# Performance work log

Hardware: AMD Instinct MI355X
Metric: run time of the kernel (lower is better)

## Reference

```python
import jax, jax.numpy as jnp
import numpy as np

M_FEATS = 1536      # number of proposals (docstring: [M, K])
K_DIM = 128         # feature dim per docstring example
NUM_CLASSES = 16    # label vocabulary; torch.unique loop becomes a fixed class sweep


def setup_inputs() -> dict:
    key = jax.random.key(0)
    k1, k2 = jax.random.split(key)
    features = jax.random.normal(k1, (M_FEATS, K_DIM), dtype=jnp.float32)
    labels = jax.random.randint(k2, (M_FEATS,), 0, NUM_CLASSES, dtype=jnp.int32)
    # ious all ones -> keep = (ious >= 0.5) is all-True, so the boolean filter is identity
    ious = jnp.ones((M_FEATS,), dtype=jnp.float32)
    return {"features": features, "labels": labels, "ious": ious}


def reference(features, labels, ious):
    # reweight_func='none' -> coef = ones_like(ious); keep mask is all-True by construction
    coef = jnp.ones_like(ious)
    # similarity [M, M]; coef broadcasts over columns, matching `similarity * coef` in torch
    sim = jnp.matmul(features, features.T) * coef[None, :]
    m = sim.shape[0]
    eye = jnp.eye(m, dtype=sim.dtype)
    # ground set term: logdet(similarity + 0.5 I)  (mask_ground is all ones)
    ground = jnp.linalg.slogdet(sim + 0.5 * eye)[1]

    # Per-label logdet of the submatrix S_c + 0.5 I_{n_c}. Instead of extracting a
    # variable-size submatrix (not jit-able), embed it in a full [M, M] matrix that is
    # block-diagonal: class block = S_c + 0.5 I, off-class diagonal = 1. Its logdet
    # equals logdet(S_c + 0.5 I). Absent classes give identity -> logdet 0, matching
    # torch.unique skipping them.
    onehot = (labels[:, None] == jnp.arange(NUM_CLASSES, dtype=labels.dtype)[None, :])
    onehot = onehot.astype(sim.dtype)  # [M, C]

    def class_logdet(mask):  # mask: [M] 0/1 indicator for one class
        A = sim * (mask[:, None] * mask[None, :]) + jnp.diag(0.5 * mask + (1.0 - mask))
        return jnp.linalg.slogdet(A)[1]

    per_class = jax.vmap(class_logdet)(onehot.T)  # [C]
    loss = jnp.sum(per_class) - ground
    return loss  # scalar; .mean() of a scalar is itself
```

## Files before the change

### kernel.cpp

```cpp
#include <hip/hip_runtime.h>
#include <math.h>


#define M_FEATS 1536
#define K_DIM 128
#define NUM_CLASSES 16
#define SLICE 96
#define GRAM_ELEMS (K_DIM * K_DIM)
#define PIDX(i) ((i) + ((i) >> 4))
#define SENT 0x13579BDF
#define MP 104

typedef short bf16x8 __attribute__((ext_vector_type(8)));
typedef float f32x4 __attribute__((ext_vector_type(4)));

__device__ __forceinline__ short f2bf(float x) {
    unsigned u = __float_as_uint(x);
    u += 0x7FFFu + ((u >> 16) & 1u);
    return (short)(u >> 16);
}

__device__ __forceinline__ void gram_mfma(
    const float* __restrict__ f, const int* list, int n, int contig_base,
    short* FT, float* __restrict__ gout, int t)
{
    const int wave = t >> 6, lane = t & 63, ln = lane & 15, quad = lane >> 4;
    const int mlane = t & 31, cgrp = t >> 5;

    f32x4 acc[2][8];
#pragma unroll
    for (int x = 0; x < 2; ++x)
#pragma unroll
        for (int tc = 0; tc < 8; ++tc)
            acc[x][tc] = (f32x4){0.f, 0.f, 0.f, 0.f};

    const int nchunks = (n + 95) / 96;
    for (int ch = 0; ch < nchunks; ++ch) {
        const int cb = ch * 96;
#pragma unroll
        for (int it = 0; it < 12; ++it) {
            const int m = (it % 3) * 32 + mlane;
            const int cg = (it / 3) * 8 + cgrp;
            const int gm = cb + m;
            float4 v = make_float4(0.f, 0.f, 0.f, 0.f);
            if (gm < n) {
                const int src = list ? list[gm] : (contig_base + gm);
                v = *(const float4*)(f + (size_t)src * K_DIM + cg * 4);
            }
            FT[(cg * 4 + 0) * MP + m] = f2bf(v.x);
            FT[(cg * 4 + 1) * MP + m] = f2bf(v.y);
            FT[(cg * 4 + 2) * MP + m] = f2bf(v.z);
            FT[(cg * 4 + 3) * MP + m] = f2bf(v.w);
        }
        __syncthreads();
#pragma unroll
        for (int kc = 0; kc < 3; ++kc) {
            const int kb = kc * 32 + quad * 8;
            bf16x8 a0 = *(const bf16x8*)(FT + ((wave * 2 + 0) * 16 + ln) * MP + kb);
            bf16x8 a1 = *(const bf16x8*)(FT + ((wave * 2 + 1) * 16 + ln) * MP + kb);
#pragma unroll
            for (int tc = 0; tc < 8; ++tc) {
                bf16x8 bb = *(const bf16x8*)(FT + (tc * 16 + ln) * MP + kb);
                acc[0][tc] = __builtin_amdgcn_mfma_f32_16x16x32_bf16(
                    a0, bb, acc[0][tc], 0, 0, 0);
                acc[1][tc] = __builtin_amdgcn_mfma_f32_16x16x32_bf16(
                    a1, bb, acc[1][tc], 0, 0, 0);
            }
        }
        __syncthreads();
    }

#pragma unroll
    for (int x = 0; x < 2; ++x)
#pragma unroll
        for (int tc = 0; tc < 8; ++tc)
#pragma unroll
            for (int rr = 0; rr < 4; ++rr)
                gout[((wave * 2 + x) * 16 + quad * 4 + rr) * K_DIM + tc * 16 + ln]
                    = acc[x][tc][rr];
}

__device__ __forceinline__ float chol128(
    float A[8][8], const int t, const int rg, const int cg,
    const int i0, const int j0,
    float4* panLo, float4* panHi, float4* wshLo, float4* wshHi, float* logp)
{
    if (rg == 0) {
#pragma unroll
        for (int q = 0; q < 8; ++q) {
            panLo[PIDX(j0 + q)] = make_float4(A[0][q], A[1][q], A[2][q], A[3][q]);
            panHi[PIDX(j0 + q)] = make_float4(A[4][q], A[5][q], A[6][q], A[7][q]);
        }
    }

#pragma unroll 1
    for (int s = 0; s < 16; ++s) {
        const int k = 8 * s;
        __syncthreads();

        if (t < K_DIM) {
            float4 dL[8], dH[8];
#pragma unroll
            for (int c = 0; c < 8; ++c) {
                dL[c] = panLo[PIDX(k + c)];
                dH[c] = panHi[PIDX(k + c)];
            }
            float4 aL = panLo[PIDX(t)], aH = panHi[PIDX(t)];

            float D[8][8];
#pragma unroll
            for (int c = 0; c < 8; ++c) {
                D[0][c] = dL[c].x; D[1][c] = dL[c].y;
                D[2][c] = dL[c].z; D[3][c] = dL[c].w;
                D[4][c] = dH[c].x; D[5][c] = dH[c].y;
                D[6][c] = dH[c].z; D[7][c] = dH[c].w;
            }

            float L[8][8], ic[8];
            float prod = 1.0f;
#pragma unroll
            for (int c = 0; c < 8; ++c) {
                float v = D[c][c];
#pragma unroll
                for (int m = 0; m < c; ++m) v = fmaf(-L[c][m], L[c][m], v);
                prod *= v;
                ic[c] = rsqrtf(v);
#pragma unroll
                for (int r = c + 1; r < 8; ++r) {
                    float x = D[r][c];
#pragma unroll
                    for (int m = 0; m < c; ++m) x = fmaf(-L[r][m], L[c][m], x);
                    L[r][c] = x * ic[c];
                }
            }
            if (t == 0) logp[s] = prod;

            float a[8] = {aL.x, aL.y, aL.z, aL.w, aH.x, aH.y, aH.z, aH.w};
            float w[8];
#pragma unroll
            for (int c = 0; c < 8; ++c) {
                float x = a[c];
#pragma unroll
                for (int m = 0; m < c; ++m) x = fmaf(-L[c][m], w[m], x);
                w[c] = x * ic[c];
            }
            wshLo[PIDX(t)] = make_float4(w[0], w[1], w[2], w[3]);
            wshHi[PIDX(t)] = make_float4(w[4], w[5], w[6], w[7]);
        }
        __syncthreads();

        if (rg > s && cg > s) {
            float4 wrL[8], wrH[8];
#pragma unroll
            for (int r = 0; r < 8; ++r) {
                wrL[r] = wshLo[PIDX(i0 + r)];
                wrH[r] = wshHi[PIDX(i0 + r)];
            }
#pragma unroll
            for (int q = 0; q < 8; ++q) {
                float4 wjL = wshLo[PIDX(j0 + q)];
                float4 wjH = wshHi[PIDX(j0 + q)];
#pragma unroll
                for (int r = 0; r < 8; ++r) {
                    float x = A[r][q];
                    x = fmaf(-wrL[r].x, wjL.x, x);
                    x = fmaf(-wrL[r].y, wjL.y, x);
                    x = fmaf(-wrL[r].z, wjL.z, x);
                    x = fmaf(-wrL[r].w, wjL.w, x);
                    x = fmaf(-wrH[r].x, wjH.x, x);
                    x = fmaf(-wrH[r].y, wjH.y, x);
                    x = fmaf(-wrH[r].z, wjH.z, x);
                    x = fmaf(-wrH[r].w, wjH.w, x);
                    A[r][q] = x;
                }
            }
        }
        if (rg == s + 1) {
#pragma unroll
            for (int q = 0; q < 8; ++q) {
                panLo[PIDX(j0 + q)] = make_float4(A[0][q], A[1][q], A[2][q], A[3][q]);
                panHi[PIDX(j0 + q)] = make_float4(A[4][q], A[5][q], A[6][q], A[7][q]);
            }
        }
    }

    float ls = 0.0f;
    if (t == 0) {
#pragma unroll
        for (int s = 0; s < 16; ++s) ls += logf(logp[s]);
    }
    return ls;
}

__global__ __launch_bounds__(256, 1) void fused_kernel(
    const float* __restrict__ f, const int* __restrict__ labels,
    float* __restrict__ partials, float* __restrict__ groundG,
    float* __restrict__ cgrams,
    int* __restrict__ flag1, int* __restrict__ flag2,
    float* __restrict__ ldet, int* __restrict__ flag3,
    float* __restrict__ out)
{
    __shared__ int cnt;
    __shared__ int list[M_FEATS];
    __shared__ short FT[K_DIM * MP];
    __shared__ float4 panLo[136], panHi[136], wshLo[136], wshHi[136];
    __shared__ float logp[16];

    const int b = blockIdx.x;
    const int t = threadIdx.x;
    const int rg = t >> 4;
    const int cg = t & 15;
    const int i0 = rg << 3;
    const int j0 = cg << 3;

    float A[8][8];

    if (b < NUM_CLASSES) {
        gram_mfma(f, nullptr, SLICE, SLICE * b, FT,
                  partials + (size_t)b * GRAM_ELEMS, t);
        __syncthreads();
        if (t == 0)
            __hip_atomic_store(&flag1[b], SENT, __ATOMIC_RELEASE,
                               __HIP_MEMORY_SCOPE_AGENT);

        if (t < NUM_CLASSES)
            while (__hip_atomic_load(&flag1[t], __ATOMIC_ACQUIRE,
                                     __HIP_MEMORY_SCOPE_AGENT) != SENT)
                __builtin_amdgcn_s_sleep(2);
        __syncthreads();

        {
            const int row = 8 * b + (t >> 5);
            const int col = (t & 31) << 2;
            float4 s = make_float4(0.f, 0.f, 0.f, 0.f);
#pragma unroll
            for (int c = 0; c < NUM_CLASSES; ++c) {
                float4 v = *(const float4*)(partials + (size_t)c * GRAM_ELEMS
                                            + row * K_DIM + col);
                s.x += v.x; s.y += v.y; s.z += v.z; s.w += v.w;
            }
            *(float4*)(groundG + row * K_DIM + col) = s;
        }
        __syncthreads();
        if (t == 0)
            __hip_atomic_store(&flag2[b], SENT, __ATOMIC_RELEASE,
                               __HIP_MEMORY_SCOPE_AGENT);
        return;
    }

    if (b < 2 * NUM_CLASSES) {
        const int cls = b - NUM_CLASSES;
        if (t == 0) cnt = 0;
        __syncthreads();
        {
            const int lane = t & 63;
            const unsigned long long ltmask = (lane == 63)
                ? 0x7FFFFFFFFFFFFFFFull : ((1ull << lane) - 1ull);
#pragma unroll
            for (int it = 0; it < M_FEATS / 256; ++it) {
                const int i = it * 256 + t;
                const bool pred = (labels[i] == cls);
                const unsigned long long mask = __ballot(pred);
                int base = 0;
                if (lane == 0 && mask)
                    base = atomicAdd(&cnt, __popcll(mask));
                base = __shfl(base, 0);
                if (pred)
                    list[base + __popcll(mask & ltmask)] = i;
            }
        }
        __syncthreads();
        const int n = cnt;

        float* g = cgrams + (size_t)cls * GRAM_ELEMS;
        gram_mfma(f, list, n, 0, FT, g, t);
        __syncthreads();

#pragma unroll
        for (int r = 0; r < 8; ++r) {
            float4 v0 = *(const float4*)(g + (i0 + r) * K_DIM + j0);
            float4 v1 = *(const float4*)(g + (i0 + r) * K_DIM + j0 + 4);
            A[r][0] = v0.x; A[r][1] = v0.y; A[r][2] = v0.z; A[r][3] = v0.w;
            A[r][4] = v1.x; A[r][5] = v1.y; A[r][6] = v1.z; A[r][7] = v1.w;
        }
#pragma unroll
        for (int r = 0; r < 8; ++r)
#pragma unroll
            for (int q = 0; q < 8; ++q)
                if ((i0 + r) == (j0 + q)) A[r][q] += 0.5f;

        float ls = chol128(A, t, rg, cg, i0, j0, panLo, panHi, wshLo, wshHi, logp);

        if (t == 0) {
            ldet[cls] = ls;
            __hip_atomic_store(&flag3[cls], SENT, __ATOMIC_RELEASE,
                               __HIP_MEMORY_SCOPE_AGENT);
        }
        return;
    }

    if (t < NUM_CLASSES)
        while (__hip_atomic_load(&flag2[t], __ATOMIC_ACQUIRE,
                                 __HIP_MEMORY_SCOPE_AGENT) != SENT)
            __builtin_amdgcn_s_sleep(2);
    __syncthreads();

#pragma unroll
    for (int r = 0; r < 8; ++r) {
        float4 v0 = *(const float4*)(groundG + (i0 + r) * K_DIM + j0);
        float4 v1 = *(const float4*)(groundG + (i0 + r) * K_DIM + j0 + 4);
        A[r][0] = v0.x; A[r][1] = v0.y; A[r][2] = v0.z; A[r][3] = v0.w;
        A[r][4] = v1.x; A[r][5] = v1.y; A[r][6] = v1.z; A[r][7] = v1.w;
    }
#pragma unroll
    for (int r = 0; r < 8; ++r)
#pragma unroll
        for (int q = 0; q < 8; ++q)
            if ((i0 + r) == (j0 + q)) A[r][q] += 0.5f;

    float ls = chol128(A, t, rg, cg, i0, j0, panLo, panHi, wshLo, wshHi, logp);

    if (t < NUM_CLASSES)
        while (__hip_atomic_load(&flag3[t], __ATOMIC_ACQUIRE,
                                 __HIP_MEMORY_SCOPE_AGENT) != SENT)
            __builtin_amdgcn_s_sleep(2);
    __syncthreads();

    if (t == 0) {
        float total = 1920.0f * 0.6931471805599453f - ls;
#pragma unroll
        for (int c = 0; c < NUM_CLASSES; ++c) total += ldet[c];
        out[0] = total;
    }
}

extern "C" void kernel_launch(void* const* d_in, const int* in_sizes, int n_in,
                              void* d_out, int out_size, void* d_ws, size_t ws_size,
                              hipStream_t stream)
{
    const float* features = (const float*)d_in[0];
    const int* labels = (const int*)d_in[1];

    float* partials = (float*)d_ws;
    float* groundG  = partials + (size_t)NUM_CLASSES * GRAM_ELEMS;
    float* cgrams   = groundG + GRAM_ELEMS;
    int* flag1      = (int*)(cgrams + (size_t)NUM_CLASSES * GRAM_ELEMS);
    int* flag2      = flag1 + NUM_CLASSES;
    float* ldetp    = (float*)(flag2 + NUM_CLASSES);
    int* flag3      = (int*)(ldetp + NUM_CLASSES);

    fused_kernel<<<2 * NUM_CLASSES + 1, 256, 0, stream>>>(
        features, labels, partials, groundG, cgrams, flag1, flag2, ldetp, flag3,
        (float*)d_out);
}
```

Measured before the change: 97.09 us.

## Use cyclic row distribution in blocked Cholesky trailing update

Rows are now assigned to thread groups cyclically (row 16*ri+rg) instead of contiguous 8-row blocks, so the trailing-matrix update stays spread across all threads as the factorization shrinks rather than idling groups whose blocks are finished. Panel publishing is rewritten to match, with each thread writing one component per step through a switch over the register row index. This adds branching on register indices and more scattered shared-memory writes, in exchange for better load balance in the 16-step factorization loop.

After: 97.63 us. About the same (+0.6%).

```diff
diff --git a/kernel.cpp b/kernel.cpp
--- a/kernel.cpp
+++ b/kernel.cpp
@@ -80,17 +80,23 @@
                     = acc[x][tc][rr];
 }
 
+#define PUBLISH_CASE(R)                                            \
+    case R: {                                                      \
+        _Pragma("unroll")                                          \
+        for (int q = 0; q < 8; ++q)                                \
+            dst[4 * PIDX(8 * cg + q) + comp] = A[R][q];            \
+    } break;
+
 __device__ __forceinline__ float chol128(
     float A[8][8], const int t, const int rg, const int cg,
-    const int i0, const int j0,
     float4* panLo, float4* panHi, float4* wshLo, float4* wshHi, float* logp)
 {
-    if (rg == 0) {
-#pragma unroll
-        for (int q = 0; q < 8; ++q) {
-            panLo[PIDX(j0 + q)] = make_float4(A[0][q], A[1][q], A[2][q], A[3][q]);
-            panHi[PIDX(j0 + q)] = make_float4(A[4][q], A[5][q], A[6][q], A[7][q]);
-        }
+    if (rg < 8) {
+        float* dst = (rg < 4) ? (float*)panLo : (float*)panHi;
+        const int comp = rg & 3;
+#pragma unroll
+        for (int q = 0; q < 8; ++q)
+            dst[4 * PIDX(8 * cg + q) + comp] = A[0][q];
     }
 
 #pragma unroll 1
@@ -122,14 +128,14 @@
             for (int c = 0; c < 8; ++c) {
                 float v = D[c][c];
 #pragma unroll
-                for (int m = 0; m < c; ++m) v = fmaf(-L[c][m], L[c][m], v);
+                for (int m2 = 0; m2 < c; ++m2) v = fmaf(-L[c][m2], L[c][m2], v);
                 prod *= v;
                 ic[c] = rsqrtf(v);
 #pragma unroll
                 for (int r = c + 1; r < 8; ++r) {
                     float x = D[r][c];
 #pragma unroll
-                    for (int m = 0; m < c; ++m) x = fmaf(-L[r][m], L[c][m], x);
+                    for (int m2 = 0; m2 < c; ++m2) x = fmaf(-L[r][m2], L[c][m2], x);
                     L[r][c] = x * ic[c];
                 }
             }
@@ -141,7 +147,7 @@
             for (int c = 0; c < 8; ++c) {
                 float x = a[c];
 #pragma unroll
-                for (int m = 0; m < c; ++m) x = fmaf(-L[c][m], w[m], x);
+                for (int m2 = 0; m2 < c; ++m2) x = fmaf(-L[c][m2], w[m2], x);
                 w[c] = x * ic[c];
             }
             wshLo[PIDX(t)] = make_float4(w[0], w[1], w[2], w[3]);
@@ -149,37 +155,43 @@
         }
         __syncthreads();
 
-        if (rg > s && cg > s) {
-            float4 wrL[8], wrH[8];
-#pragma unroll
-            for (int r = 0; r < 8; ++r) {
-                wrL[r] = wshLo[PIDX(i0 + r)];
-                wrH[r] = wshHi[PIDX(i0 + r)];
-            }
+        const int m = (s + 1) >> 1;
+        if (m < 8) {
+            float4 wjL[8], wjH[8];
 #pragma unroll
             for (int q = 0; q < 8; ++q) {
-                float4 wjL = wshLo[PIDX(j0 + q)];
-                float4 wjH = wshHi[PIDX(j0 + q)];
-#pragma unroll
-                for (int r = 0; r < 8; ++r) {
-                    float x = A[r][q];
-                    x = fmaf(-wrL[r].x, wjL.x, x);
-                    x = fmaf(-wrL[r].y, wjL.y, x);
-                    x = fmaf(-wrL[r].z, wjL.z, x);
-                    x = fmaf(-wrL[r].w, wjL.w, x);
-                    x = fmaf(-wrH[r].x, wjH.x, x);
-                    x = fmaf(-wrH[r].y, wjH.y, x);
-                    x = fmaf(-wrH[r].z, wjH.z, x);
-                    x = fmaf(-wrH[r].w, wjH.w, x);
-                    A[r][q] = x;
+                wjL[q] = wshLo[PIDX(8 * cg + q)];
+                wjH[q] = wshHi[PIDX(8 * cg + q)];
+            }
+#pragma unroll
+            for (int ri = 0; ri < 8; ++ri) {
+                if (ri >= m) {
+                    float4 wrL = wshLo[PIDX(16 * ri + rg)];
+                    float4 wrH = wshHi[PIDX(16 * ri + rg)];
+#pragma unroll
+                    for (int q = 0; q < 8; ++q) {
+                        float x = A[ri][q];
+                        x = fmaf(-wrL.x, wjL[q].x, x);
+                        x = fmaf(-wrL.y, wjL[q].y, x);
+                        x = fmaf(-wrL.z, wjL[q].z, x);
+                        x = fmaf(-wrL.w, wjL[q].w, x);
+                        x = fmaf(-wrH.x, wjH[q].x, x);
+                        x = fmaf(-wrH.y, wjH[q].y, x);
+                        x = fmaf(-wrH.z, wjH[q].z, x);
+                        x = fmaf(-wrH.w, wjH[q].w, x);
+                        A[ri][q] = x;
+                    }
                 }
             }
         }
-        if (rg == s + 1) {
-#pragma unroll
-            for (int q = 0; q < 8; ++q) {
-                panLo[PIDX(j0 + q)] = make_float4(A[0][q], A[1][q], A[2][q], A[3][q]);
-                panHi[PIDX(j0 + q)] = make_float4(A[4][q], A[5][q], A[6][q], A[7][q]);
+
+        if (s < 15 && (rg >> 3) == ((s + 1) & 1)) {
+            const int rip = rg & 7;
+            float* dst = (rip < 4) ? (float*)panLo : (float*)panHi;
+            const int comp = rip & 3;
+            switch ((s + 1) >> 1) {
+                PUBLISH_CASE(0) PUBLISH_CASE(1) PUBLISH_CASE(2) PUBLISH_CASE(3)
+                PUBLISH_CASE(4) PUBLISH_CASE(5) PUBLISH_CASE(6) PUBLISH_CASE(7)
             }
         }
     }
@@ -190,6 +202,24 @@
         for (int s = 0; s < 16; ++s) ls += logf(logp[s]);
     }
     return ls;
+}
+
+__device__ __forceinline__ void load_tiles(
+    const float* __restrict__ g, float A[8][8], int rg, int cg)
+{
+#pragma unroll
+    for (int ri = 0; ri < 8; ++ri) {
+        const int r = 16 * ri + rg;
+        float4 v0 = *(const float4*)(g + r * K_DIM + 8 * cg);
+        float4 v1 = *(const float4*)(g + r * K_DIM + 8 * cg + 4);
+        A[ri][0] = v0.x; A[ri][1] = v0.y; A[ri][2] = v0.z; A[ri][3] = v0.w;
+        A[ri][4] = v1.x; A[ri][5] = v1.y; A[ri][6] = v1.z; A[ri][7] = v1.w;
+    }
+#pragma unroll
+    for (int ri = 0; ri < 8; ++ri)
+#pragma unroll
+        for (int q = 0; q < 8; ++q)
+            if ((16 * ri + rg) == (8 * cg + q)) A[ri][q] += 0.5f;
 }
 
 __global__ __launch_bounds__(256, 1) void fused_kernel(
@@ -210,8 +240,6 @@
     const int t = threadIdx.x;
     const int rg = t >> 4;
     const int cg = t & 15;
-    const int i0 = rg << 3;
-    const int j0 = cg << 3;
 
     float A[8][8];
 
@@ -276,20 +304,8 @@
         gram_mfma(f, list, n, 0, FT, g, t);
         __syncthreads();
 
-#pragma unroll
-        for (int r = 0; r < 8; ++r) {
-            float4 v0 = *(const float4*)(g + (i0 + r) * K_DIM + j0);
-            float4 v1 = *(const float4*)(g + (i0 + r) * K_DIM + j0 + 4);
-            A[r][0] = v0.x; A[r][1] = v0.y; A[r][2] = v0.z; A[r][3] = v0.w;
-            A[r][4] = v1.x; A[r][5] = v1.y; A[r][6] = v1.z; A[r][7] = v1.w;
-        }
-#pragma unroll
-        for (int r = 0; r < 8; ++r)
-#pragma unroll
-            for (int q = 0; q < 8; ++q)
-                if ((i0 + r) == (j0 + q)) A[r][q] += 0.5f;
-
-        float ls = chol128(A, t, rg, cg, i0, j0, panLo, panHi, wshLo, wshHi, logp);
+        load_tiles(g, A, rg, cg);
+        float ls = chol128(A, t, rg, cg, panLo, panHi, wshLo, wshHi, logp);
 
         if (t == 0) {
             ldet[cls] = ls;
@@ -305,20 +321,8 @@
             __builtin_amdgcn_s_sleep(2);
     __syncthreads();
 
-#pragma unroll
-    for (int r = 0; r < 8; ++r) {
-        float4 v0 = *(const float4*)(groundG + (i0 + r) * K_DIM + j0);
-        float4 v1 = *(const float4*)(groundG + (i0 + r) * K_DIM + j0 + 4);
-        A[r][0] = v0.x; A[r][1] = v0.y; A[r][2] = v0.z; A[r][3] = v0.w;
-        A[r][4] = v1.x; A[r][5] = v1.y; A[r][6] = v1.z; A[r][7] = v1.w;
-    }
-#pragma unroll
-    for (int r = 0; r < 8; ++r)
-#pragma unroll
-        for (int q = 0; q < 8; ++q)
-            if ((i0 + r) == (j0 + q)) A[r][q] += 0.5f;
-
-    float ls = chol128(A, t, rg, cg, i0, j0, panLo, panHi, wshLo, wshHi, logp);
+    load_tiles(groundG, A, rg, cg);
+    float ls = chol128(A, t, rg, cg, panLo, panHi, wshLo, wshHi, logp);
 
     if (t < NUM_CLASSES)
         while (__hip_atomic_load(&flag3[t], __ATOMIC_ACQUIRE,
```
